# Performance work log

Measured on AMD Instinct MI355X. Metric: run time of the kernel, lower is better.

Reference implementation:

```python
import jax, jax.numpy as jnp
import numpy as np

S, FRAME, CLS, D, HWA, HWV, DOUT = 32, 8, 32, 512, 8, 14, 128


def setup_inputs() -> dict:
    key = jax.random.key(0)
    ks = jax.random.split(key, 12)
    rng = np.random.default_rng(0)
    # per-(segment,class) random permutation of frames (torch.randperm(frame))
    rand_frames = np.stack([rng.permutation(FRAME) for _ in range(S * CLS)]).reshape(S, CLS, FRAME).astype(np.int32)
    rand_classes = rng.integers(0, CLS, size=(S, CLS, FRAME)).astype(np.int32)
    return {
        "feat_a": jax.random.normal(ks[0], (S * CLS, D, HWA, HWA), jnp.float32),
        "pred_a": jax.random.uniform(ks[1], (S, CLS), jnp.float32),
        "feat_v": jax.random.normal(ks[2], (S * FRAME, D, HWV, HWV), jnp.float32),
        "pred_v": jax.random.normal(ks[3], (S * FRAME, CLS), jnp.float32),
        "cam": jax.random.uniform(ks[4], (S * FRAME, CLS, 1, HWV, HWV), jnp.float32),
        "rand_frames": jnp.asarray(rand_frames),
        "rand_classes": jnp.asarray(rand_classes),
        "Wt": jax.random.normal(ks[5], (D, D), jnp.float32) * (1.0 / np.sqrt(D)),
        "bt": jnp.zeros((D,), jnp.float32),
        "Ws": jax.random.normal(ks[6], (D, D), jnp.float32) * (1.0 / np.sqrt(D)),
        "bs": jnp.zeros((D,), jnp.float32),
        "Wa": jax.random.normal(ks[7], (DOUT, D), jnp.float32) * (1.0 / np.sqrt(D)),
        "ba": jnp.zeros((DOUT,), jnp.float32),
        "Wv": jax.random.normal(ks[8], (DOUT, D), jnp.float32) * (1.0 / np.sqrt(D)),
        "bv": jnp.zeros((DOUT,), jnp.float32),
    }


def reference(feat_a, pred_a, feat_v, pred_v, cam, rand_frames, rand_classes,
              Wt, bt, Ws, bs, Wa, ba, Wv, bv):
    S_, C_ = pred_a.shape
    F_ = pred_v.shape[0] // S_

    # temp_conv (1x1) + AdaptiveMaxPool2d(1,1): max over H,W (bias is per-channel const)
    ca = jnp.einsum('bihw,oi->bohw', feat_a, Wt)  # [S*C, D, H, W]
    fa = ca.max(axis=(2, 3)) + bt                 # [S*C, D]
    fa = fa.reshape(S_, C_, -1)                   # [S, C, D]

    # spa_conv (1x1) then cam-weighted foreground pooling (fg branch of cam_pool)
    cv = jnp.einsum('bihw,oi->bohw', feat_v, Ws) + bs[None, :, None, None]  # [S*F, D, H, W]
    camq = cam[:, :, 0]                                                     # [S*F, C, H, W]
    fg = jnp.einsum('bdhw,bchw->bcd', cv, camq)
    fg = fg / (camq.sum(axis=(2, 3))[..., None] + 1e-10)                    # [S*F, C, D]
    fg = fg.reshape(S_, F_, C_, -1)                                         # [S, F, C, D]

    pv = jax.nn.sigmoid(pred_v.reshape(S_, F_, C_))
    active_a = pred_a > 0.3            # [S, C]  (index_a; the chained-index line is a no-op)
    active_v = pv > 0.3                # [S, F, C] (eff_v membership)

    # transforms
    ta = fa @ Wa.T + ba                                    # [S, C, DOUT]
    tv = jnp.einsum('sfcd,od->sfco', fg, Wv) + bv          # [S, F, C, DOUT]

    # 'same' pairs: (seg, frame, class) where both audio class and video frame-class fire
    mask_co = (active_a[:, None, :] & active_v)            # [S, F, C]
    loss_co = ((ta[:, None, :, :] - tv) ** 2).mean(-1)     # [S, F, C]
    loss_co = jnp.transpose(loss_co, (0, 2, 1)) * jnp.transpose(mask_co, (0, 2, 1))  # [S, C, F]

    # 'differ' pairs: num = int(pred_a*frame) random (frame,class) picks from partner seg
    num = (pred_a * F_).astype(jnp.int32)                  # [S, C]
    mask_di = active_a[:, :, None] & (jnp.arange(F_)[None, None, :] < num[:, :, None])  # [S, C, F]
    rank = jnp.arange(S_) ^ 1                              # seg+1 if even else seg-1
    tv_di = tv[rank[:, None, None], rand_frames, rand_classes]  # [S, C, F, DOUT]
    loss_di = ((ta[:, :, None, :] - tv_di) ** 2).mean(-1) * mask_di  # [S, C, F]

    # dense masked layout of (embed_co, embed_di); invalid slots are exactly 0
    return jnp.stack([loss_co, loss_di])  # [2, S, C, F]
```

## Files before the change

### kernel.cpp

```cpp
#include <hip/hip_runtime.h>


typedef __attribute__((ext_vector_type(8))) short bf16x8;
typedef __attribute__((ext_vector_type(4))) float f32x4;

__device__ __forceinline__ unsigned short f2bf(float x) {
    union { float f; unsigned u; } v; v.f = x;
    unsigned r = v.u + 0x7FFFu + ((v.u >> 16) & 1u);
    return (unsigned short)(r >> 16);
}
__device__ __forceinline__ unsigned pk2(float a, float b) {
    return (unsigned)f2bf(a) | ((unsigned)f2bf(b) << 16);
}

__global__ __launch_bounds__(256) void k0_wtbf(
    const float* __restrict__ Wt, unsigned short* __restrict__ Wt_bf)
{
    int i = blockIdx.x * 256 + threadIdx.x;
    float4 v = ((const float4*)Wt)[i];
    *(unsigned*)&Wt_bf[i*4]     = pk2(v.x, v.y);
    *(unsigned*)&Wt_bf[i*4 + 2] = pk2(v.z, v.w);
}

__global__ __launch_bounds__(256, 2) void k1_fa(
    const float* __restrict__ feat_a, const unsigned short* __restrict__ Wt_bf,
    const float* __restrict__ bt, float* __restrict__ fa)
{
    __shared__ unsigned short lds_b[64 * 512];
    const int b = blockIdx.x, t = threadIdx.x;
    const int w = t >> 6, l = t & 63, lo = l & 15, hi = l >> 4;

    const float* fb = feat_a + (size_t)b * 512 * 64;
    const int hw = l;
#pragma unroll 2
    for (int it = 0; it < 16; ++it) {
        int koct = it * 4 + w;
        float v[8];
#pragma unroll
        for (int j = 0; j < 8; ++j)
            v[j] = fb[(koct * 8 + j) * 64 + hw];
        unsigned u[4];
#pragma unroll
        for (int j = 0; j < 4; ++j) u[j] = pk2(v[2*j], v[2*j + 1]);
        int chunk = koct ^ (hw & 7);
        *(uint4*)((char*)lds_b + hw * 1024 + chunk * 16) = *(uint4*)u;
    }
    __syncthreads();

    f32x4 acc[8][4];
#pragma unroll
    for (int i = 0; i < 8; ++i)
#pragma unroll
        for (int j = 0; j < 4; ++j) acc[i][j] = (f32x4)(0.f);
    const int o0 = w * 128;
    for (int ks = 0; ks < 16; ++ks) {
        bf16x8 bfr[4];
#pragma unroll
        for (int nf = 0; nf < 4; ++nf) {
            int ko = ks * 4 + hi;
            int chunk = ko ^ (lo & 7);
            bfr[nf] = *(const bf16x8*)((char*)lds_b + (nf*16 + lo) * 1024 + chunk * 16);
        }
#pragma unroll
        for (int mo = 0; mo < 8; ++mo) {
            bf16x8 afr = *(const bf16x8*)&Wt_bf[(o0 + mo*16 + lo) * 512 + ks*32 + hi*8];
#pragma unroll
            for (int nf = 0; nf < 4; ++nf)
                acc[mo][nf] = __builtin_amdgcn_mfma_f32_16x16x32_bf16(afr, bfr[nf], acc[mo][nf], 0, 0, 0);
        }
    }
#pragma unroll
    for (int mo = 0; mo < 8; ++mo)
#pragma unroll
        for (int reg = 0; reg < 4; ++reg) {
            float m = fmaxf(fmaxf(acc[mo][0][reg], acc[mo][1][reg]),
                            fmaxf(acc[mo][2][reg], acc[mo][3][reg]));
            m = fmaxf(m, __shfl_xor(m, 1));
            m = fmaxf(m, __shfl_xor(m, 2));
            m = fmaxf(m, __shfl_xor(m, 4));
            m = fmaxf(m, __shfl_xor(m, 8));
            if (lo == 0) {
                int orow = o0 + mo*16 + hi*4 + reg;
                fa[(size_t)b * 512 + orow] = m + bt[orow];
            }
        }
}

__global__ __launch_bounds__(256) void k2_g(
    const float* __restrict__ feat_v, const float* __restrict__ cam,
    unsigned short* __restrict__ g_bf, float* __restrict__ camsum)
{
    __shared__ unsigned short cam_s[32][232];
    __shared__ unsigned short feat_s[64][232];
    const int half = blockIdx.x, b = blockIdx.y, t = threadIdx.x;
    const int w = t >> 6, l = t & 63, lo = l & 15, hi = l >> 4;

    const float* camb = &cam[b * 32 * 196];
    for (int i4 = t; i4 < 1568; i4 += 256) {
        int c = i4 / 49, h4 = (i4 - c*49) * 4;
        float4 v = ((const float4*)camb)[i4];
        *(unsigned*)&cam_s[c][h4]     = pk2(v.x, v.y);
        *(unsigned*)&cam_s[c][h4 + 2] = pk2(v.z, v.w);
    }
    for (int idx = t; idx < 32*28; idx += 256) {
        int c = idx / 28, hh = 196 + (idx - c*28);
        cam_s[c][hh] = 0;
    }
    if (half == 0) {
        int c = t >> 3, seg = t & 7;
        int h0 = seg * 25, h1 = min(196, h0 + 25);
        float s = 0.f;
        const float* p = &camb[c * 196];
        for (int q = h0; q < h1; ++q) s += p[q];
        s += __shfl_xor(s, 1);
        s += __shfl_xor(s, 2);
        s += __shfl_xor(s, 4);
        if (seg == 0) camsum[b*32 + c] = s;
    }

    for (int ic = half*4; ic < half*4 + 4; ++ic) {
        __syncthreads();
        const float* fbv = &feat_v[((size_t)b*512 + ic*64) * 196];
        for (int i4 = t; i4 < 3136; i4 += 256) {
            int r = i4 / 49, h4 = (i4 - r*49) * 4;
            float4 v = ((const float4*)fbv)[i4];
            *(unsigned*)&feat_s[r][h4]     = pk2(v.x, v.y);
            *(unsigned*)&feat_s[r][h4 + 2] = pk2(v.z, v.w);
        }
        for (int idx = t; idx < 64*28; idx += 256) {
            int r = idx / 28, hh = 196 + (idx - r*28);
            feat_s[r][hh] = 0;
        }
        __syncthreads();
        f32x4 acc[2]; acc[0] = (f32x4)(0.f); acc[1] = (f32x4)(0.f);
#pragma unroll
        for (int kt = 0; kt < 7; ++kt) {
            bf16x8 a0 = *(const bf16x8*)&cam_s[lo][kt*32 + hi*8];
            bf16x8 a1 = *(const bf16x8*)&cam_s[16 + lo][kt*32 + hi*8];
            bf16x8 bb = *(const bf16x8*)&feat_s[w*16 + lo][kt*32 + hi*8];
            acc[0] = __builtin_amdgcn_mfma_f32_16x16x32_bf16(a0, bb, acc[0], 0, 0, 0);
            acc[1] = __builtin_amdgcn_mfma_f32_16x16x32_bf16(a1, bb, acc[1], 0, 0, 0);
        }
#pragma unroll
        for (int mo = 0; mo < 2; ++mo)
#pragma unroll
            for (int reg = 0; reg < 4; ++reg) {
                int c = mo*16 + hi*4 + reg;
                int i = ic*64 + w*16 + lo;
                g_bf[((size_t)b*32 + c)*512 + i] = f2bf(acc[mo][reg]);
            }
    }
}

__global__ __launch_bounds__(256) void k3_wvs(
    const float* __restrict__ Wv, const float* __restrict__ Ws, const float* __restrict__ bs,
    unsigned short* __restrict__ Wvs_bf, float* __restrict__ wvbs)
{
    __shared__ float red[256];
    const int o = blockIdx.x, t = threadIdx.x;
    float a0 = 0.f, a1 = 0.f;
    for (int d = 0; d < 512; ++d) {
        float wv = Wv[o*512 + d];
        a0 += wv * Ws[d*512 + t];
        a1 += wv * Ws[d*512 + t + 256];
    }
    Wvs_bf[o*512 + t]       = f2bf(a0);
    Wvs_bf[o*512 + t + 256] = f2bf(a1);
    red[t] = Wv[o*512 + t] * bs[t] + Wv[o*512 + t + 256] * bs[t + 256];
    __syncthreads();
    for (int s2 = 128; s2 > 0; s2 >>= 1) {
        if (t < s2) red[t] += red[t + s2];
        __syncthreads();
    }
    if (t == 0) wvbs[o] = red[0];
}

__global__ __launch_bounds__(64) void k4_tv(
    const unsigned short* __restrict__ g_bf, const unsigned short* __restrict__ Wvs_bf,
    const float* __restrict__ camsum, const float* __restrict__ wvbs,
    const float* __restrict__ bv, float* __restrict__ tv)
{
    const int m0 = blockIdx.x * 32;
    const int l = threadIdx.x, lo = l & 15, hi = l >> 4;
    f32x4 acc[2][8];
#pragma unroll
    for (int i = 0; i < 2; ++i)
#pragma unroll
        for (int j = 0; j < 8; ++j) acc[i][j] = (f32x4)(0.f);
    for (int k0 = 0; k0 < 512; k0 += 32) {
        bf16x8 a0 = *(const bf16x8*)&g_bf[(m0 + lo)*512 + k0 + hi*8];
        bf16x8 a1 = *(const bf16x8*)&g_bf[(m0 + 16 + lo)*512 + k0 + hi*8];
#pragma unroll
        for (int nf = 0; nf < 8; ++nf) {
            bf16x8 bb = *(const bf16x8*)&Wvs_bf[(nf*16 + lo)*512 + k0 + hi*8];
            acc[0][nf] = __builtin_amdgcn_mfma_f32_16x16x32_bf16(a0, bb, acc[0][nf], 0, 0, 0);
            acc[1][nf] = __builtin_amdgcn_mfma_f32_16x16x32_bf16(a1, bb, acc[1][nf], 0, 0, 0);
        }
    }
#pragma unroll
    for (int mo = 0; mo < 2; ++mo)
#pragma unroll
        for (int reg = 0; reg < 4; ++reg) {
            int bc = m0 + mo*16 + hi*4 + reg;
            float cs = camsum[bc];
            float inv = 1.f / (cs + 1e-10f);
#pragma unroll
            for (int nf = 0; nf < 8; ++nf) {
                int o = nf*16 + lo;
                tv[bc*128 + o] = (acc[mo][nf][reg] + cs * wvbs[o]) * inv + bv[o];
            }
        }
}

__global__ __launch_bounds__(128) void k5_ta(
    const float* __restrict__ fa, const float* __restrict__ Wa,
    const float* __restrict__ ba, float* __restrict__ ta)
{
    __shared__ float fa_s[4 * 512];
    const int r0 = blockIdx.x * 4, t = threadIdx.x;
    for (int j = t; j < 512; j += 128)
        ((float4*)fa_s)[j] = ((const float4*)&fa[r0 * 512])[j];
    __syncthreads();
    float acc[4];
#pragma unroll
    for (int r = 0; r < 4; ++r) acc[r] = 0.f;
    const float4* wa4 = (const float4*)&Wa[t * 512];
    for (int j = 0; j < 128; ++j) {
        float4 wv = wa4[j];
#pragma unroll
        for (int r = 0; r < 4; ++r) {
            float4 fv = ((const float4*)&fa_s[r * 512])[j];
            acc[r] += wv.x*fv.x + wv.y*fv.y + wv.z*fv.z + wv.w*fv.w;
        }
    }
    float bao = ba[t];
#pragma unroll
    for (int r = 0; r < 4; ++r) ta[(r0 + r)*128 + t] = acc[r] + bao;
}

__global__ __launch_bounds__(256) void k6_loss(
    const float* __restrict__ ta, const float* __restrict__ tv,
    const float* __restrict__ pred_a, const float* __restrict__ pred_v,
    const int* __restrict__ rand_frames, const int* __restrict__ rand_classes,
    float* __restrict__ out)
{
    const int blk = blockIdx.x;
    const int s = blk >> 5, c = blk & 31;
    const int t = threadIdx.x, w = t >> 6, l = t & 63;
    const float ta0 = ta[blk*128 + l], ta1 = ta[blk*128 + 64 + l];
    const float pa = pred_a[blk];
    const bool aa = pa > 0.3f;
    const int num = (int)(pa * 8.0f);
    const float LOGIT03 = -0.84729786f;
#pragma unroll
    for (int ff = 0; ff < 2; ++ff) {
        int f = w*2 + ff;
        int row = (s*8 + f)*32 + c;
        float d0 = ta0 - tv[row*128 + l];
        float d1 = ta1 - tv[row*128 + 64 + l];
        float ss = d0*d0 + d1*d1;
        for (int m = 32; m > 0; m >>= 1) ss += __shfl_xor(ss, m);
        bool av = pred_v[(s*8 + f)*32 + c] > LOGIT03;
        if (l == 0) out[blk*8 + f] = (aa && av) ? ss * (1.f/128.f) : 0.f;
        int fi = rand_frames[blk*8 + f];
        int ci = rand_classes[blk*8 + f];
        int row2 = ((s ^ 1)*8 + fi)*32 + ci;
        float e0 = ta0 - tv[row2*128 + l];
        float e1 = ta1 - tv[row2*128 + 64 + l];
        float s2 = e0*e0 + e1*e1;
        for (int m = 32; m > 0; m >>= 1) s2 += __shfl_xor(s2, m);
        if (l == 0) out[8192 + blk*8 + f] = (aa && (f < num)) ? s2 * (1.f/128.f) : 0.f;
    }
}

extern "C" void kernel_launch(void* const* d_in, const int* in_sizes, int n_in,
                              void* d_out, int out_size, void* d_ws, size_t ws_size,
                              hipStream_t stream) {
    const float* feat_a = (const float*)d_in[0];
    const float* pred_a = (const float*)d_in[1];
    const float* feat_v = (const float*)d_in[2];
    const float* pred_v = (const float*)d_in[3];
    const float* cam    = (const float*)d_in[4];
    const int* rand_frames  = (const int*)d_in[5];
    const int* rand_classes = (const int*)d_in[6];
    const float* Wt = (const float*)d_in[7];
    const float* bt = (const float*)d_in[8];
    const float* Ws = (const float*)d_in[9];
    const float* bs = (const float*)d_in[10];
    const float* Wa = (const float*)d_in[11];
    const float* ba = (const float*)d_in[12];
    const float* Wv = (const float*)d_in[13];
    const float* bv = (const float*)d_in[14];
    float* out = (float*)d_out;

    char* ws = (char*)d_ws;
    float* fa              = (float*)(ws + 0);
    float* ta              = (float*)(ws + 2097152);
    unsigned short* Wt_bf  = (unsigned short*)(ws + 2097152);
    unsigned short* g_bf   = (unsigned short*)(ws + 2621440);
    float* camsum          = (float*)(ws + 11010048);
    unsigned short* Wvs_bf = (unsigned short*)(ws + 11042816);
    float* wvbs            = (float*)(ws + 11173888);
    float* tv              = (float*)(ws + 11174400);

    k0_wtbf<<<256, 256, 0, stream>>>(Wt, Wt_bf);
    k3_wvs<<<128, 256, 0, stream>>>(Wv, Ws, bs, Wvs_bf, wvbs);
    k1_fa<<<1024, 256, 0, stream>>>(feat_a, Wt_bf, bt, fa);
    k2_g<<<dim3(2, 256), 256, 0, stream>>>(feat_v, cam, g_bf, camsum);
    k4_tv<<<256, 64, 0, stream>>>(g_bf, Wvs_bf, camsum, wvbs, bv, tv);
    k5_ta<<<256, 128, 0, stream>>>(fa, Wa, ba, ta);
    k6_loss<<<1024, 256, 0, stream>>>(ta, tv, pred_a, pred_v, rand_frames, rand_classes, out);
}
```

Measured before the change: 460.9 us.

## Pre-swizzle weights into MFMA fragment layout and widen blocks across kernels

Weights Wt and Wv·Ws are now stored in an MFMA-fragment-ordered layout, so each lane does one contiguous 16-byte load instead of strided row reads. k1 and k2 move to 512 threads, with each wave doing less work. k2 double-buffers the feat_v staging so the next chunk loads while the current one computes. k3 and k4 are split across more blocks and waves to raise parallelism. The cost is more register pressure and launch-bound tuning that may hurt occupancy in k1.

```diff
diff --git a/kernel.cpp b/kernel.cpp
--- a/kernel.cpp
+++ b/kernel.cpp
@@ -13,28 +13,31 @@
     return (unsigned)f2bf(a) | ((unsigned)f2bf(b) << 16);
 }
 
-__global__ __launch_bounds__(256) void k0_wtbf(
-    const float* __restrict__ Wt, unsigned short* __restrict__ Wt_bf)
-{
-    int i = blockIdx.x * 256 + threadIdx.x;
-    float4 v = ((const float4*)Wt)[i];
-    *(unsigned*)&Wt_bf[i*4]     = pk2(v.x, v.y);
-    *(unsigned*)&Wt_bf[i*4 + 2] = pk2(v.z, v.w);
-}
-
-__global__ __launch_bounds__(256, 2) void k1_fa(
-    const float* __restrict__ feat_a, const unsigned short* __restrict__ Wt_bf,
+__global__ __launch_bounds__(256) void k0_wtf(
+    const float* __restrict__ Wt, unsigned short* __restrict__ WtF)
+{
+    int g = blockIdx.x * 256 + threadIdx.x;
+    int ot = g >> 10, ks = (g >> 6) & 15, l = g & 63;
+    int lo = l & 15, hi = l >> 4;
+    const float* src = &Wt[(ot*16 + lo) * 512 + ks*32 + hi*8];
+    float4 f0 = ((const float4*)src)[0], f1 = ((const float4*)src)[1];
+    uint4 u = { pk2(f0.x,f0.y), pk2(f0.z,f0.w), pk2(f1.x,f1.y), pk2(f1.z,f1.w) };
+    *(uint4*)&WtF[(size_t)g * 8] = u;
+}
+
+__global__ __launch_bounds__(512, 4) void k1_fa(
+    const float* __restrict__ feat_a, const unsigned short* __restrict__ WtF,
     const float* __restrict__ bt, float* __restrict__ fa)
 {
     __shared__ unsigned short lds_b[64 * 512];
     const int b = blockIdx.x, t = threadIdx.x;
     const int w = t >> 6, l = t & 63, lo = l & 15, hi = l >> 4;
 
-    const float* fb = feat_a + (size_t)b * 512 * 64;
+    const float* fb = feat_a + (size_t)b * 32768;
     const int hw = l;
 #pragma unroll 2
-    for (int it = 0; it < 16; ++it) {
-        int koct = it * 4 + w;
+    for (int it = 0; it < 8; ++it) {
+        int koct = it * 8 + w;
         float v[8];
 #pragma unroll
         for (int j = 0; j < 8; ++j)
@@ -47,30 +50,30 @@
     }
     __syncthreads();
 
-    f32x4 acc[8][4];
-#pragma unroll
-    for (int i = 0; i < 8; ++i)
+    f32x4 acc[4][4];
+#pragma unroll
+    for (int i = 0; i < 4; ++i)
 #pragma unroll
         for (int j = 0; j < 4; ++j) acc[i][j] = (f32x4)(0.f);
-    const int o0 = w * 128;
+    const unsigned short* wtf = WtF + (size_t)(w * 4) * 8192;
     for (int ks = 0; ks < 16; ++ks) {
         bf16x8 bfr[4];
 #pragma unroll
         for (int nf = 0; nf < 4; ++nf) {
-            int ko = ks * 4 + hi;
-            int chunk = ko ^ (lo & 7);
+            int chunk = (ks * 4 + hi) ^ (lo & 7);
             bfr[nf] = *(const bf16x8*)((char*)lds_b + (nf*16 + lo) * 1024 + chunk * 16);
         }
 #pragma unroll
-        for (int mo = 0; mo < 8; ++mo) {
-            bf16x8 afr = *(const bf16x8*)&Wt_bf[(o0 + mo*16 + lo) * 512 + ks*32 + hi*8];
+        for (int mo = 0; mo < 4; ++mo) {
+            bf16x8 afr = *(const bf16x8*)&wtf[(size_t)((mo*16 + ks)*64 + l) * 8];
 #pragma unroll
             for (int nf = 0; nf < 4; ++nf)
                 acc[mo][nf] = __builtin_amdgcn_mfma_f32_16x16x32_bf16(afr, bfr[nf], acc[mo][nf], 0, 0, 0);
         }
     }
-#pragma unroll
-    for (int mo = 0; mo < 8; ++mo)
+    const int o0 = w * 64;
+#pragma unroll
+    for (int mo = 0; mo < 4; ++mo)
 #pragma unroll
         for (int reg = 0; reg < 4; ++reg) {
             float m = fmaxf(fmaxf(acc[mo][0][reg], acc[mo][1][reg]),
@@ -86,115 +89,117 @@
         }
 }
 
-__global__ __launch_bounds__(256) void k2_g(
+__global__ __launch_bounds__(512) void k2_g(
     const float* __restrict__ feat_v, const float* __restrict__ cam,
     unsigned short* __restrict__ g_bf, float* __restrict__ camsum)
 {
     __shared__ unsigned short cam_s[32][232];
-    __shared__ unsigned short feat_s[64][232];
+    __shared__ unsigned short feat_s[2][64][232];
     const int half = blockIdx.x, b = blockIdx.y, t = threadIdx.x;
     const int w = t >> 6, l = t & 63, lo = l & 15, hi = l >> 4;
-
-    const float* camb = &cam[b * 32 * 196];
-    for (int i4 = t; i4 < 1568; i4 += 256) {
+    const int mo = w >> 2, nf = w & 3;
+
+    const float* camb = &cam[b * 6272];
+    for (int i4 = t; i4 < 1568; i4 += 512) {
         int c = i4 / 49, h4 = (i4 - c*49) * 4;
         float4 v = ((const float4*)camb)[i4];
         *(unsigned*)&cam_s[c][h4]     = pk2(v.x, v.y);
         *(unsigned*)&cam_s[c][h4 + 2] = pk2(v.z, v.w);
     }
-    for (int idx = t; idx < 32*28; idx += 256) {
-        int c = idx / 28, hh = 196 + (idx - c*28);
-        cam_s[c][hh] = 0;
+    for (int idx = t; idx < 32*28; idx += 512) {
+        int c = idx / 28; cam_s[c][196 + (idx - c*28)] = 0;
+    }
+    for (int idx = t; idx < 2*64*28; idx += 512) {
+        int bu = idx / 1792, r = (idx - bu*1792) / 28, hh = 196 + (idx % 28);
+        feat_s[bu][r][hh] = 0;
     }
     if (half == 0) {
-        int c = t >> 3, seg = t & 7;
-        int h0 = seg * 25, h1 = min(196, h0 + 25);
+        int c = t >> 4, seg = l & 15;
+        int h0 = seg * 13, h1 = min(196, h0 + 13);
         float s = 0.f;
         const float* p = &camb[c * 196];
         for (int q = h0; q < h1; ++q) s += p[q];
-        s += __shfl_xor(s, 1);
-        s += __shfl_xor(s, 2);
-        s += __shfl_xor(s, 4);
+        s += __shfl_xor(s, 1); s += __shfl_xor(s, 2);
+        s += __shfl_xor(s, 4); s += __shfl_xor(s, 8);
         if (seg == 0) camsum[b*32 + c] = s;
     }
 
-    for (int ic = half*4; ic < half*4 + 4; ++ic) {
-        __syncthreads();
+    auto STAGE = [&](int ic, int bu) {
         const float* fbv = &feat_v[((size_t)b*512 + ic*64) * 196];
-        for (int i4 = t; i4 < 3136; i4 += 256) {
+        for (int i4 = t; i4 < 3136; i4 += 512) {
             int r = i4 / 49, h4 = (i4 - r*49) * 4;
             float4 v = ((const float4*)fbv)[i4];
-            *(unsigned*)&feat_s[r][h4]     = pk2(v.x, v.y);
-            *(unsigned*)&feat_s[r][h4 + 2] = pk2(v.z, v.w);
-        }
-        for (int idx = t; idx < 64*28; idx += 256) {
-            int r = idx / 28, hh = 196 + (idx - r*28);
-            feat_s[r][hh] = 0;
+            *(unsigned*)&feat_s[bu][r][h4]     = pk2(v.x, v.y);
+            *(unsigned*)&feat_s[bu][r][h4 + 2] = pk2(v.z, v.w);
+        }
+    };
+    STAGE(half*4, 0);
+    __syncthreads();
+    for (int q = 0; q < 4; ++q) {
+        int ic = half*4 + q;
+        if (q < 3) STAGE(ic + 1, (q + 1) & 1);
+        f32x4 acc = (f32x4)(0.f);
+#pragma unroll
+        for (int kt = 0; kt < 7; ++kt) {
+            bf16x8 a  = *(const bf16x8*)&cam_s[mo*16 + lo][kt*32 + hi*8];
+            bf16x8 bb = *(const bf16x8*)&feat_s[q & 1][nf*16 + lo][kt*32 + hi*8];
+            acc = __builtin_amdgcn_mfma_f32_16x16x32_bf16(a, bb, acc, 0, 0, 0);
+        }
+#pragma unroll
+        for (int reg = 0; reg < 4; ++reg) {
+            int c = mo*16 + hi*4 + reg;
+            int i = ic*64 + nf*16 + lo;
+            g_bf[((size_t)b*32 + c)*512 + i] = f2bf(acc[reg]);
         }
         __syncthreads();
-        f32x4 acc[2]; acc[0] = (f32x4)(0.f); acc[1] = (f32x4)(0.f);
-#pragma unroll
-        for (int kt = 0; kt < 7; ++kt) {
-            bf16x8 a0 = *(const bf16x8*)&cam_s[lo][kt*32 + hi*8];
-            bf16x8 a1 = *(const bf16x8*)&cam_s[16 + lo][kt*32 + hi*8];
-            bf16x8 bb = *(const bf16x8*)&feat_s[w*16 + lo][kt*32 + hi*8];
-            acc[0] = __builtin_amdgcn_mfma_f32_16x16x32_bf16(a0, bb, acc[0], 0, 0, 0);
-            acc[1] = __builtin_amdgcn_mfma_f32_16x16x32_bf16(a1, bb, acc[1], 0, 0, 0);
-        }
-#pragma unroll
-        for (int mo = 0; mo < 2; ++mo)
-#pragma unroll
-            for (int reg = 0; reg < 4; ++reg) {
-                int c = mo*16 + hi*4 + reg;
-                int i = ic*64 + w*16 + lo;
-                g_bf[((size_t)b*32 + c)*512 + i] = f2bf(acc[mo][reg]);
-            }
     }
 }
 
 __global__ __launch_bounds__(256) void k3_wvs(
     const float* __restrict__ Wv, const float* __restrict__ Ws, const float* __restrict__ bs,
-    unsigned short* __restrict__ Wvs_bf, float* __restrict__ wvbs)
+    unsigned short* __restrict__ WvsF, float* __restrict__ wvbs)
 {
     __shared__ float red[256];
-    const int o = blockIdx.x, t = threadIdx.x;
-    float a0 = 0.f, a1 = 0.f;
-    for (int d = 0; d < 512; ++d) {
-        float wv = Wv[o*512 + d];
-        a0 += wv * Ws[d*512 + t];
-        a1 += wv * Ws[d*512 + t + 256];
-    }
-    Wvs_bf[o*512 + t]       = f2bf(a0);
-    Wvs_bf[o*512 + t + 256] = f2bf(a1);
-    red[t] = Wv[o*512 + t] * bs[t] + Wv[o*512 + t + 256] * bs[t + 256];
-    __syncthreads();
-    for (int s2 = 128; s2 > 0; s2 >>= 1) {
-        if (t < s2) red[t] += red[t + s2];
+    const int o = blockIdx.x >> 1, ih = blockIdx.x & 1, t = threadIdx.x;
+    const int i = ih*256 + t;
+    float a0 = 0.f;
+#pragma unroll 4
+    for (int d = 0; d < 512; ++d)
+        a0 += Wv[o*512 + d] * Ws[d*512 + i];
+    int nf = o >> 4, lo2 = o & 15, ks = i >> 5, hi2 = (i >> 3) & 3, j = i & 7;
+    WvsF[(size_t)(((nf*16 + ks)*64) + hi2*16 + lo2)*8 + j] = f2bf(a0);
+    if (ih == 0) {
+        red[t] = Wv[o*512 + t]*bs[t] + Wv[o*512 + t + 256]*bs[t + 256];
         __syncthreads();
-    }
-    if (t == 0) wvbs[o] = red[0];
-}
-
-__global__ __launch_bounds__(64) void k4_tv(
-    const unsigned short* __restrict__ g_bf, const unsigned short* __restrict__ Wvs_bf,
+        for (int s2 = 128; s2 > 0; s2 >>= 1) {
+            if (t < s2) red[t] += red[t + s2];
+            __syncthreads();
+        }
+        if (t == 0) wvbs[o] = red[0];
+    }
+}
+
+__global__ __launch_bounds__(256) void k4_tv(
+    const unsigned short* __restrict__ g_bf, const unsigned short* __restrict__ WvsF,
     const float* __restrict__ camsum, const float* __restrict__ wvbs,
     const float* __restrict__ bv, float* __restrict__ tv)
 {
     const int m0 = blockIdx.x * 32;
-    const int l = threadIdx.x, lo = l & 15, hi = l >> 4;
-    f32x4 acc[2][8];
+    const int t = threadIdx.x, w = t >> 6, l = t & 63, lo = l & 15, hi = l >> 4;
+    f32x4 acc[2][2];
 #pragma unroll
     for (int i = 0; i < 2; ++i)
 #pragma unroll
-        for (int j = 0; j < 8; ++j) acc[i][j] = (f32x4)(0.f);
-    for (int k0 = 0; k0 < 512; k0 += 32) {
-        bf16x8 a0 = *(const bf16x8*)&g_bf[(m0 + lo)*512 + k0 + hi*8];
-        bf16x8 a1 = *(const bf16x8*)&g_bf[(m0 + 16 + lo)*512 + k0 + hi*8];
-#pragma unroll
-        for (int nf = 0; nf < 8; ++nf) {
-            bf16x8 bb = *(const bf16x8*)&Wvs_bf[(nf*16 + lo)*512 + k0 + hi*8];
-            acc[0][nf] = __builtin_amdgcn_mfma_f32_16x16x32_bf16(a0, bb, acc[0][nf], 0, 0, 0);
-            acc[1][nf] = __builtin_amdgcn_mfma_f32_16x16x32_bf16(a1, bb, acc[1][nf], 0, 0, 0);
+        for (int j = 0; j < 2; ++j) acc[i][j] = (f32x4)(0.f);
+    for (int ks = 0; ks < 16; ++ks) {
+        bf16x8 a0 = *(const bf16x8*)&g_bf[(size_t)(m0 + lo)*512 + ks*32 + hi*8];
+        bf16x8 a1 = *(const bf16x8*)&g_bf[(size_t)(m0 + 16 + lo)*512 + ks*32 + hi*8];
+#pragma unroll
+        for (int nn = 0; nn < 2; ++nn) {
+            int nf = w*2 + nn;
+            bf16x8 bb = *(const bf16x8*)&WvsF[(size_t)((nf*16 + ks)*64 + l) * 8];
+            acc[0][nn] = __builtin_amdgcn_mfma_f32_16x16x32_bf16(a0, bb, acc[0][nn], 0, 0, 0);
+            acc[1][nn] = __builtin_amdgcn_mfma_f32_16x16x32_bf16(a1, bb, acc[1][nn], 0, 0, 0);
         }
     }
 #pragma unroll
@@ -205,9 +210,9 @@
             float cs = camsum[bc];
             float inv = 1.f / (cs + 1e-10f);
 #pragma unroll
-            for (int nf = 0; nf < 8; ++nf) {
-                int o = nf*16 + lo;
-                tv[bc*128 + o] = (acc[mo][nf][reg] + cs * wvbs[o]) * inv + bv[o];
+            for (int nn = 0; nn < 2; ++nn) {
+                int o = (w*2 + nn)*16 + lo;
+                tv[(size_t)bc*128 + o] = (acc[mo][nn][reg] + cs * wvbs[o]) * inv + bv[o];
             }
         }
 }
@@ -225,6 +230,7 @@
 #pragma unroll
     for (int r = 0; r < 4; ++r) acc[r] = 0.f;
     const float4* wa4 = (const float4*)&Wa[t * 512];
+#pragma unroll 4
     for (int j = 0; j < 128; ++j) {
         float4 wv = wa4[j];
 #pragma unroll
@@ -296,18 +302,18 @@
     char* ws = (char*)d_ws;
     float* fa              = (float*)(ws + 0);
     float* ta              = (float*)(ws + 2097152);
-    unsigned short* Wt_bf  = (unsigned short*)(ws + 2097152);
+    unsigned short* WtF    = (unsigned short*)(ws + 2097152);
     unsigned short* g_bf   = (unsigned short*)(ws + 2621440);
     float* camsum          = (float*)(ws + 11010048);
-    unsigned short* Wvs_bf = (unsigned short*)(ws + 11042816);
+    unsigned short* WvsF   = (unsigned short*)(ws + 11042816);
     float* wvbs            = (float*)(ws + 11173888);
     float* tv              = (float*)(ws + 11174400);
 
-    k0_wtbf<<<256, 256, 0, stream>>>(Wt, Wt_bf);
-    k3_wvs<<<128, 256, 0, stream>>>(Wv, Ws, bs, Wvs_bf, wvbs);
-    k1_fa<<<1024, 256, 0, stream>>>(feat_a, Wt_bf, bt, fa);
-    k2_g<<<dim3(2, 256), 256, 0, stream>>>(feat_v, cam, g_bf, camsum);
-    k4_tv<<<256, 64, 0, stream>>>(g_bf, Wvs_bf, camsum, wvbs, bv, tv);
+    k0_wtf<<<128, 256, 0, stream>>>(Wt, WtF);
+    k3_wvs<<<256, 256, 0, stream>>>(Wv, Ws, bs, WvsF, wvbs);
+    k1_fa<<<1024, 512, 0, stream>>>(feat_a, WtF, bt, fa);
+    k2_g<<<dim3(2, 256), 512, 0, stream>>>(feat_v, cam, g_bf, camsum);
+    k4_tv<<<256, 256, 0, stream>>>(g_bf, WvsF, camsum, wvbs, bv, tv);
     k5_ta<<<256, 128, 0, stream>>>(fa, Wa, ba, ta);
     k6_loss<<<1024, 256, 0, stream>>>(ta, tv, pred_a, pred_v, rand_frames, rand_classes, out);
 }
```

Result: faster. 422.8 us (-8.3%).
